# Performance work log

Measured on AMD Instinct MI355X. Metric: run time of the kernel, lower is better.

The kernel has to match this reference:

```python
import jax, jax.numpy as jnp
import numpy as np

B, S, D, H = 2, 2048, 2048, 16
HD = D // H
SCALE = 1.0 / np.sqrt(HD)


def setup_inputs() -> dict:
    key = jax.random.key(0)
    ks = jax.random.split(key, 11)
    xav = np.sqrt(6.0 / (D + D))  # xavier uniform bound for square weights
    def w(k):
        return jax.random.uniform(k, (D, D), jnp.float32, -xav, xav)
    return {
        "query": jax.random.normal(ks[0], (B, S, D), jnp.float32),
        "key": jax.random.normal(ks[1], (B, S, D), jnp.float32),
        "value": jax.random.normal(ks[2], (B, S, D), jnp.float32),
        "Wq": w(ks[3]), "bq": jnp.zeros((D,), jnp.float32),
        "Wk": w(ks[4]), "bk": jnp.zeros((D,), jnp.float32),
        "Wv": w(ks[5]), "bv": jnp.zeros((D,), jnp.float32),
        "Wo": w(ks[6]), "bo": jnp.zeros((D,), jnp.float32),
    }


def reference(query, key, value, Wq, bq, Wk, bk, Wv, bv, Wo, bo):
    # projections (torch Linear: x @ W.T + b)
    q = query @ Wq.T + bq
    k = key @ Wk.T + bk
    v = value @ Wv.T + bv
    # [B, H, S, HD]
    q = q.reshape(B, S, H, HD).transpose(0, 2, 1, 3)
    k = k.reshape(B, S, H, HD).transpose(0, 2, 1, 3)
    v = v.reshape(B, S, H, HD).transpose(0, 2, 1, 3)
    scores = jnp.einsum("bhqd,bhkd->bhqk", q, k) * SCALE
    causal = jnp.triu(jnp.ones((S, S), bool), k=1)
    scores = jnp.where(causal, -jnp.inf, scores)
    attn = jax.nn.softmax(scores, axis=-1)  # dropout p=0.0 -> identity
    out = jnp.einsum("bhqk,bhkd->bhqd", attn, v)
    out = out.transpose(0, 2, 1, 3).reshape(B, S, D)
    return out @ Wo.T + bo
```

## Files before the change

### kernel.cpp

```cpp
#include <hip/hip_runtime.h>
#include <hip/hip_bf16.h>


#define LOG2E 1.44269504088896340736f

typedef __attribute__((ext_vector_type(8))) short short8;
typedef __attribute__((ext_vector_type(4))) short short4b;
typedef __attribute__((ext_vector_type(4))) float floatx4;

__device__ __forceinline__ short f2bf(float f) {
  unsigned int u = __builtin_bit_cast(unsigned int, f);
  u += 0x7FFFu + ((u >> 16) & 1u);
  return (short)(u >> 16);
}

__device__ __forceinline__ short8 cvt8(float4 f0, float4 f1) {
  return (short8){f2bf(f0.x), f2bf(f0.y), f2bf(f0.z), f2bf(f0.w),
                  f2bf(f1.x), f2bf(f1.y), f2bf(f1.z), f2bf(f1.w)};
}

__device__ __forceinline__ short4b pack4bf(float a, float b, float c, float d) {
  __hip_bfloat162 lo = __float22bfloat162_rn(float2{a, b});
  __hip_bfloat162 hi = __float22bfloat162_rn(float2{c, d});
  short4b r;
  r[0] = __builtin_bit_cast(short, lo.x); r[1] = __builtin_bit_cast(short, lo.y);
  r[2] = __builtin_bit_cast(short, hi.x); r[3] = __builtin_bit_cast(short, hi.y);
  return r;
}

__device__ __forceinline__ void gl_lds16(const void* g, void* l) {
  __builtin_amdgcn_global_load_lds(
      (const __attribute__((address_space(1))) unsigned int*)g,
      (__attribute__((address_space(3))) unsigned int*)l, 16, 0, 0);
}

__global__ __launch_bounds__(256) void cvt7_k(
    const float* __restrict__ s0, const float* __restrict__ s1,
    const float* __restrict__ s2, const float* __restrict__ s3,
    const float* __restrict__ s4, const float* __restrict__ s5,
    const float* __restrict__ s6,
    unsigned short* __restrict__ d0, unsigned short* __restrict__ d1,
    unsigned short* __restrict__ d2, unsigned short* __restrict__ d3,
    unsigned short* __restrict__ d4, unsigned short* __restrict__ d5,
    unsigned short* __restrict__ d6, int nAct, int nW)
{
  const float* s; unsigned short* d; int n;
  switch (blockIdx.y) {
    case 0: s = s0; d = d0; n = nAct; break;
    case 1: s = s1; d = d1; n = nAct; break;
    case 2: s = s2; d = d2; n = nAct; break;
    case 3: s = s3; d = d3; n = nW; break;
    case 4: s = s4; d = d4; n = nW; break;
    case 5: s = s5; d = d5; n = nW; break;
    default: s = s6; d = d6; n = nW; break;
  }
  const long i = ((long)blockIdx.x * 256 + threadIdx.x) * 8;
  if (i >= n) return;
  float4 a = *(const float4*)(s + i);
  float4 b = *(const float4*)(s + i + 4);
  *(short8*)(d + i) = cvt8(a, b);
}

#define GEMM_CORE(A_, Bt_)                                                     \
  const unsigned short* gA[4]; int lAo[4];                                     \
  const unsigned short* gB[2]; int lBo[2];                                     \
  _Pragma("unroll")                                                            \
  for (int j = 0; j < 4; ++j) {                                                \
    const int pa = ((j >> 1) * 16 + wave * 2 + (j & 1)) * 64 + lane;           \
    const int r = pa >> 3, cp = pa & 7, cs = cp ^ (r & 7);                     \
    gA[j]  = A_ + (bm + r) * (long)K + cs * 8;                                 \
    lAo[j] = pa * 8;                                                           \
  }                                                                            \
  _Pragma("unroll")                                                            \
  for (int j = 0; j < 2; ++j) {                                                \
    const int pb = (wave * 2 + j) * 64 + lane;                                 \
    const int r = pb >> 3, cp = pb & 7, cs = cp ^ (r & 7);                     \
    gB[j]  = Bt_ + (bn + r) * (long)K + cs * 8;                                \
    lBo[j] = pb * 8;                                                           \
  }                                                                            \
  floatx4 acc[4][4];                                                           \
  _Pragma("unroll")                                                            \
  for (int i = 0; i < 4; ++i)                                                  \
    _Pragma("unroll")                                                          \
    for (int j = 0; j < 4; ++j) acc[i][j] = (floatx4){0.f, 0.f, 0.f, 0.f};     \
  const int NT = K >> 6;                                                       \
  _Pragma("unroll")                                                            \
  for (int j = 0; j < 4; ++j) gl_lds16(gA[j], &As[0][lAo[j]]);                 \
  _Pragma("unroll")                                                            \
  for (int j = 0; j < 2; ++j) gl_lds16(gB[j], &Bs[0][lBo[j]]);                 \
  if (NT > 1) {                                                                \
    _Pragma("unroll")                                                          \
    for (int j = 0; j < 4; ++j) gl_lds16(gA[j] + 64, &As[1][lAo[j]]);          \
    _Pragma("unroll")                                                          \
    for (int j = 0; j < 2; ++j) gl_lds16(gB[j] + 64, &Bs[1][lBo[j]]);          \
    asm volatile("s_waitcnt vmcnt(6)" ::: "memory");                           \
  } else {                                                                     \
    asm volatile("s_waitcnt vmcnt(0)" ::: "memory");                           \
  }                                                                            \
  __builtin_amdgcn_s_barrier();                                                \
  int cur3 = 0;                                                                \
  for (int t = 0; t < NT; ++t) {                                               \
    int nx2 = cur3 + 2; if (nx2 >= 3) nx2 -= 3;                                \
    const long kk2 = (long)(t + 2) * 64;                                       \
    const bool st2 = (t + 2) < NT;                                             \
    const bool st1 = (t + 1) < NT;                                             \
    const unsigned short* Ab = As[cur3];                                       \
    const unsigned short* Bb = Bs[cur3];                                       \
                            \
    short8 af0[4], bf0[4], af1[4], bf1[4];                                     \
    _Pragma("unroll")                                                          \
    for (int mt = 0; mt < 4; ++mt)                                             \
      af0[mt] = *(const short8*)&Ab[(wm * 64 + mt * 16 + l16) * 64 +           \
                                    ((quad ^ lx7) * 8)];                       \
    _Pragma("unroll")                                                          \
    for (int nt = 0; nt < 4; ++nt)                                             \
      bf0[nt] = *(const short8*)&Bb[(wn * 64 + nt * 16 + l16) * 64 +           \
                                    ((quad ^ lx7) * 8)];                       \
    _Pragma("unroll")                                                          \
    for (int mt = 0; mt < 4; ++mt)                                             \
      af1[mt] = *(const short8*)&Ab[(wm * 64 + mt * 16 + l16) * 64 +           \
                                    (((4 + quad) ^ lx7) * 8)];                 \
    _Pragma("unroll")                                                          \
    for (int nt = 0; nt < 4; ++nt)                                             \
      bf1[nt] = *(const short8*)&Bb[(wn * 64 + nt * 16 + l16) * 64 +           \
                                    (((4 + quad) ^ lx7) * 8)];                 \
    if (st2) { gl_lds16(gA[0] + kk2, &As[nx2][lAo[0]]);                        \
               gl_lds16(gA[1] + kk2, &As[nx2][lAo[1]]);                        \
               gl_lds16(gA[2] + kk2, &As[nx2][lAo[2]]); }                      \
    __builtin_amdgcn_s_barrier();                                              \
                      \
    __builtin_amdgcn_s_setprio(1);                                             \
    _Pragma("unroll")                                                          \
    for (int nt = 0; nt < 4; ++nt)                                             \
      _Pragma("unroll")                                                        \
      for (int mt = 0; mt < 4; ++mt)                                           \
        acc[mt][nt] = __builtin_amdgcn_mfma_f32_16x16x32_bf16(                 \
            af0[mt], bf0[nt], acc[mt][nt], 0, 0, 0);                           \
    __builtin_amdgcn_s_setprio(0);                                             \
    __builtin_amdgcn_s_barrier();                                              \
                         \
    if (st2) { gl_lds16(gA[3] + kk2, &As[nx2][lAo[3]]);                        \
               gl_lds16(gB[0] + kk2, &Bs[nx2][lBo[0]]);                        \
               gl_lds16(gB[1] + kk2, &Bs[nx2][lBo[1]]); }                      \
    __builtin_amdgcn_s_setprio(1);                                             \
    _Pragma("unroll")                                                          \
    for (int nt = 0; nt < 4; ++nt)                                             \
      _Pragma("unroll")                                                        \
      for (int mt = 0; mt < 4; ++mt)                                           \
        acc[mt][nt] = __builtin_amdgcn_mfma_f32_16x16x32_bf16(                 \
            af1[mt], bf1[nt], acc[mt][nt], 0, 0, 0);                           \
    __builtin_amdgcn_s_setprio(0);                                             \
    if (st1) {                                                                 \
      if (st2) asm volatile("s_waitcnt vmcnt(6)" ::: "memory");                \
      else     asm volatile("s_waitcnt vmcnt(0)" ::: "memory");                \
    }                                                                          \
    __builtin_amdgcn_s_barrier();                                              \
    cur3 = cur3 + 1 >= 3 ? 0 : cur3 + 1;                                       \
  }

__global__ __launch_bounds__(512, 1) void gemmqkv_k(
    const unsigned short* __restrict__ Aq, const unsigned short* __restrict__ Ak,
    const unsigned short* __restrict__ Av,
    const unsigned short* __restrict__ Bq, const unsigned short* __restrict__ Bk,
    const unsigned short* __restrict__ Bv,
    const float* __restrict__ biq, const float* __restrict__ bik,
    const float* __restrict__ biv,
    unsigned short* __restrict__ Cq, unsigned short* __restrict__ Ck,
    unsigned short* __restrict__ Cv, float qalpha)
{
  constexpr int K = 2048, N = 2048;
  __shared__ __align__(16) unsigned short As[3][256 * 64];
  __shared__ __align__(16) unsigned short Bs[3][128 * 64];

  const int tid  = threadIdx.x;
  const int lane = tid & 63;
  const int wave = tid >> 6;
  const int quad = lane >> 4;
  const int l16  = lane & 15;
  const int lx7  = l16 & 7;
  const int wm   = wave >> 1, wn = wave & 1;

  const unsigned short* A; const unsigned short* Bt; const float* bias;
  unsigned short* C; float alpha = 1.0f; bool vt = false;
  if (blockIdx.z == 0)      { A = Aq; Bt = Bq; bias = biq; C = Cq; alpha = qalpha; }
  else if (blockIdx.z == 1) { A = Ak; Bt = Bk; bias = bik; C = Ck; }
  else                      { A = Av; Bt = Bv; bias = biv; C = Cv; vt = true; }

  const int lin  = (int)(blockIdx.y * 16 + blockIdx.x);
  const int xcd  = lin & 7;
  const int slot = lin >> 3;
  const int bx = (xcd & 1) * 8 + (slot & 7);
  const int by = (xcd >> 1) * 4 + (slot >> 3);
  const long bm = (long)by * 256;
  const long bn = (long)bx * 128;

  GEMM_CORE(A, Bt)

  if (vt) {
    __syncthreads();
    unsigned short* Ct = &As[0][0];
#pragma unroll
    for (int nt = 0; nt < 4; ++nt) {
      const int col_l = wn * 64 + nt * 16 + l16;
      const float bval = bias[bn + col_l];
#pragma unroll
      for (int mt = 0; mt < 4; ++mt) {
        const int row_l = wm * 64 + mt * 16 + quad * 4;
#pragma unroll
        for (int rg = 0; rg < 4; ++rg)
          Ct[col_l * 264 + row_l + rg] = (unsigned short)f2bf((acc[mt][nt][rg] + bval) * alpha);
      }
    }
    __syncthreads();
    const int b  = (int)(bm >> 11);
    const int s0 = (int)(bm & 2047);
    const int d   = tid >> 2;
    const int seg = tid & 3;
    unsigned short* dst = C +
        ((long)(b * 16 + bx) * 128 + d) * 2048 + s0 + seg * 64;
    const unsigned short* src = &Ct[d * 264 + seg * 64];
#pragma unroll
    for (int c = 0; c < 8; ++c)
      *(uint4*)(dst + c * 8) = *(const uint4*)(src + c * 8);
  } else {
#pragma unroll
    for (int nt = 0; nt < 4; ++nt) {
      const long col = bn + wn * 64 + nt * 16 + l16;
      const float bval = bias[col];
#pragma unroll
      for (int mt = 0; mt < 4; ++mt) {
#pragma unroll
        for (int rg = 0; rg < 4; ++rg) {
          const long row = bm + wm * 64 + mt * 16 + quad * 4 + rg;
          C[row * (long)N + col] = (unsigned short)f2bf((acc[mt][nt][rg] + bval) * alpha);
        }
      }
    }
  }
}

__global__ __launch_bounds__(512, 1) void gemmo_k(
    const unsigned short* __restrict__ A, const unsigned short* __restrict__ Bt,
    const float* __restrict__ bias, float* __restrict__ C)
{
  constexpr int K = 2048, N = 2048;
  __shared__ __align__(16) unsigned short As[3][256 * 64];
  __shared__ __align__(16) unsigned short Bs[3][128 * 64];

  const int tid  = threadIdx.x;
  const int lane = tid & 63;
  const int wave = tid >> 6;
  const int quad = lane >> 4;
  const int l16  = lane & 15;
  const int lx7  = l16 & 7;
  const int wm   = wave >> 1, wn = wave & 1;

  const int lin  = (int)(blockIdx.y * 16 + blockIdx.x);
  const int xcd  = lin & 7;
  const int slot = lin >> 3;
  const int bx = (xcd & 1) * 8 + (slot & 7);
  const int by = (xcd >> 1) * 4 + (slot >> 3);
  const long bm = (long)by * 256;
  const long bn = (long)bx * 128;

  GEMM_CORE(A, Bt)

#pragma unroll
  for (int nt = 0; nt < 4; ++nt) {
    const long col = bn + wn * 64 + nt * 16 + l16;
    const float bval = bias[col];
#pragma unroll
    for (int mt = 0; mt < 4; ++mt) {
#pragma unroll
      for (int rg = 0; rg < 4; ++rg) {
        const long row = bm + wm * 64 + mt * 16 + quad * 4 + rg;
        C[row * (long)N + col] = (acc[mt][nt][rg] + bval);
      }
    }
  }
}

template<bool A_BF16, bool OUT_BF16, bool VT_OUT>
__global__ __launch_bounds__(256, 2) void gemm_bias_k(
    const void* __restrict__ Aptr, const float* __restrict__ Bt,
    const float* __restrict__ bias, void* __restrict__ Cptr,
    int M, int N, int K, float alpha)
{
  __shared__ __align__(16) unsigned short smem[128 * 136];
  unsigned short* As = smem;
  unsigned short* Bs = smem + 128 * 40;

  const int tid  = threadIdx.x;
  const int lane = tid & 63;
  const int wave = tid >> 6;
  const int quad = lane >> 4;
  const int l16  = lane & 15;
  const int wr   = wave >> 1, wc = wave & 1;
  const long bm  = (long)blockIdx.y * 128;
  const long bn  = (long)blockIdx.x * 128;

  floatx4 acc[4][4];
#pragma unroll
  for (int i = 0; i < 4; ++i)
#pragma unroll
    for (int j = 0; j < 4; ++j) acc[i][j] = (floatx4){0.f, 0.f, 0.f, 0.f};

  const int srow = tid >> 2;
  const int cc   = tid & 3;

  for (int k0 = 0; k0 < K; k0 += 32) {
    __syncthreads();
#pragma unroll
    for (int r = 0; r < 2; ++r) {
      const int row = srow + r * 64;
      short8 av, bv;
      if (A_BF16) {
        av = *(const short8*)((const unsigned short*)Aptr + (bm + row) * (long)K + k0 + cc * 8);
      } else {
        const float* ap = (const float*)Aptr + (bm + row) * (long)K + k0 + cc * 8;
        av = cvt8(*(const float4*)ap, *(const float4*)(ap + 4));
      }
      {
        const float* bp = Bt + (bn + row) * (long)K + k0 + cc * 8;
        bv = cvt8(*(const float4*)bp, *(const float4*)(bp + 4));
      }
      *(short8*)&As[row * 40 + cc * 8] = av;
      *(short8*)&Bs[row * 40 + cc * 8] = bv;
    }
    __syncthreads();

    short8 af[4], bf[4];
#pragma unroll
    for (int t = 0; t < 4; ++t) {
      af[t] = *(const short8*)&As[(wr * 64 + t * 16 + l16) * 40 + quad * 8];
      bf[t] = *(const short8*)&Bs[(wc * 64 + t * 16 + l16) * 40 + quad * 8];
    }
#pragma unroll
    for (int mt = 0; mt < 4; ++mt)
#pragma unroll
      for (int nt = 0; nt < 4; ++nt)
        acc[mt][nt] = __builtin_amdgcn_mfma_f32_16x16x32_bf16(af[mt], bf[nt], acc[mt][nt], 0, 0, 0);
  }

  if (VT_OUT) {
    __syncthreads();
    unsigned short* Ct = smem;
#pragma unroll
    for (int nt = 0; nt < 4; ++nt) {
      const long col = bn + wc * 64 + nt * 16 + l16;
      const float bval = bias[col];
      const int col_l = wc * 64 + nt * 16 + l16;
#pragma unroll
      for (int mt = 0; mt < 4; ++mt) {
        const int row_l = wr * 64 + mt * 16 + quad * 4;
#pragma unroll
        for (int rg = 0; rg < 4; ++rg)
          Ct[col_l * 136 + row_l + rg] = (unsigned short)f2bf((acc[mt][nt][rg] + bval) * alpha);
      }
    }
    __syncthreads();
    const int b  = (int)(bm >> 11);
    const int s0 = (int)(bm & 2047);
    const int r    = tid >> 1;
    const int half = tid & 1;
    unsigned short* dst = (unsigned short*)Cptr +
        ((long)(b * 16 + blockIdx.x) * 128 + r) * 2048 + s0 + half * 64;
    const unsigned short* src = &Ct[r * 136 + half * 64];
#pragma unroll
    for (int c = 0; c < 8; ++c)
      *(uint4*)(dst + c * 8) = *(const uint4*)(src + c * 8);
  } else {
#pragma unroll
    for (int nt = 0; nt < 4; ++nt) {
      const long col = bn + wc * 64 + nt * 16 + l16;
      const float bval = bias[col];
#pragma unroll
      for (int mt = 0; mt < 4; ++mt) {
#pragma unroll
        for (int rg = 0; rg < 4; ++rg) {
          const long row = bm + wr * 64 + mt * 16 + quad * 4 + rg;
          const float v = (acc[mt][nt][rg] + bval) * alpha;
          if (OUT_BF16) ((unsigned short*)Cptr)[row * (long)N + col] = (unsigned short)f2bf(v);
          else          ((float*)Cptr)[row * (long)N + col] = v;
        }
      }
    }
  }
}

__global__ __launch_bounds__(256, 2) void flash_attn_k(
    const unsigned short* __restrict__ Q,
    const unsigned short* __restrict__ Kp,
    const unsigned short* __restrict__ Vt,
    unsigned short* __restrict__ O)
{
  constexpr int S = 2048, D = 2048, HD = 128;
  constexpr int PS = 72;

  __shared__ __align__(16) unsigned short Ks[2][64 * 128];
  __shared__ __align__(16) unsigned short Vst[2][128 * 64];
  __shared__ __align__(16) unsigned short Ps[64 * PS];

  const int tid  = threadIdx.x;
  const int lane = tid & 63;
  const int w    = tid >> 6;
  const int quad = lane >> 4;
  const int l16  = lane & 15;
  const int lx7  = l16 & 7;

  const int bx  = blockIdx.x;
  const int by  = blockIdx.y;
  const int idx = by * 2 + (bx >> 3);
  const int bh  = (bx & 7) * 4 + (idx >> 4);
  const int qsel = idx & 15;

  const long headoff = (long)(bh >> 4) * S * D + (long)(bh & 15) * HD;
  const long vtoff   = (long)bh * HD * S;

  const unsigned short* gK[4]; int oK[4];
  const unsigned short* gV[4]; int oV[4];
#pragma unroll
  for (int i = 0; i < 4; ++i) {
    const int p = (w * 4 + i) * 64 + lane;
    { const int r = p >> 4, cp = p & 15, c = cp ^ (r & 7);
      gK[i] = Kp + headoff + (long)r * D + c * 8;  oK[i] = p * 8; }
    { const int r = p >> 3, cp = p & 7, c = cp ^ (r & 7);
      gV[i] = Vt + vtoff + (long)r * S + c * 8;    oV[i] = p * 8; }
  }

#pragma unroll 1
  for (int half = 0; half < 2; ++half) {
    const int qt = half ? (31 - qsel) : qsel;
    const int qbase = qt * 64;
    const int qrow  = qbase + w * 16 + l16;
    const int qloc  = w * 16 + l16;

    short8 aq[4];
    {
      const unsigned short* qp = Q + headoff + (long)qrow * D;
#pragma unroll
      for (int ks = 0; ks < 4; ++ks)
        aq[ks] = *(const short8*)(qp + ks * 32 + quad * 8);
    }

    floatx4 o_acc[8];
#pragma unroll
    for (int t = 0; t < 8; ++t) o_acc[t] = (floatx4){0.f, 0.f, 0.f, 0.f};
    float m_i = -INFINITY;
    float l_p = 0.f;

#pragma unroll
    for (int i = 0; i < 4; ++i) gl_lds16(gK[i], &Ks[0][oK[i]]);
#pragma unroll
    for (int i = 0; i < 4; ++i) gl_lds16(gV[i], &Vst[0][oV[i]]);

    for (int kt = 0; kt <= qt; ++kt) {
      const int cur = kt & 1;
      const int kbase = kt * 64;
      if (kt < qt) {
        const long kb = (long)(kt + 1) * 64;
        const int nb = cur ^ 1;
#pragma unroll
        for (int i = 0; i < 4; ++i) gl_lds16(gK[i] + kb * D, &Ks[nb][oK[i]]);
#pragma unroll
        for (int i = 0; i < 4; ++i) gl_lds16(gV[i] + kb, &Vst[nb][oV[i]]);
        asm volatile("s_waitcnt vmcnt(8)" ::: "memory");
      } else {
        asm volatile("s_waitcnt vmcnt(0)" ::: "memory");
      }
      __builtin_amdgcn_s_barrier();

      const unsigned short* Kb = &Ks[cur][0];
      const unsigned short* Vb = &Vst[cur][0];

      floatx4 sc[4];
#pragma unroll
      for (int nt = 0; nt < 4; ++nt) sc[nt] = (floatx4){0.f, 0.f, 0.f, 0.f};
      __builtin_amdgcn_s_setprio(1);
#pragma unroll
      for (int nt = 0; nt < 4; ++nt) {
        const int krow = nt * 16 + l16;
#pragma unroll
        for (int ks = 0; ks < 4; ++ks) {
          const int cp = (ks * 4 + quad) ^ lx7;
          short8 kf = *(const short8*)&Kb[krow * 128 + cp * 8];
          sc[nt] = __builtin_amdgcn_mfma_f32_16x16x32_bf16(kf, aq[ks], sc[nt], 0, 0, 0);
        }
      }
      __builtin_amdgcn_s_setprio(0);

      float sv[4][4];
      float lmax = -INFINITY;
      if (kt == qt) {
        const int kg0 = kbase + quad * 4;
#pragma unroll
        for (int nt = 0; nt < 4; ++nt)
#pragma unroll
          for (int rg = 0; rg < 4; ++rg) {
            float v = sc[nt][rg];
            if (kg0 + nt * 16 + rg > qrow) v = -INFINITY;
            sv[nt][rg] = v;
            lmax = fmaxf(lmax, v);
          }
      } else {
#pragma unroll
        for (int nt = 0; nt < 4; ++nt)
#pragma unroll
          for (int rg = 0; rg < 4; ++rg) {
            sv[nt][rg] = sc[nt][rg];
            lmax = fmaxf(lmax, sc[nt][rg]);
          }
      }

      float al = 1.0f;
      if (__any(lmax > m_i + 8.0f)) {
        float rmax = fmaxf(lmax, __shfl_xor(lmax, 16));
        rmax = fmaxf(rmax, __shfl_xor(rmax, 32));
        const float mn = fmaxf(m_i, rmax);
        al = exp2f(m_i - mn);
        m_i = mn;
#pragma unroll
        for (int t = 0; t < 8; ++t)
#pragma unroll
          for (int rg = 0; rg < 4; ++rg) o_acc[t][rg] *= al;
      }

      float rsum = 0.f;
#pragma unroll
      for (int nt = 0; nt < 4; ++nt) {
        float p0 = exp2f(sv[nt][0] - m_i), p1 = exp2f(sv[nt][1] - m_i);
        float p2 = exp2f(sv[nt][2] - m_i), p3 = exp2f(sv[nt][3] - m_i);
        rsum += (p0 + p1) + (p2 + p3);
        *(short4b*)&Ps[qloc * PS + nt * 16 + quad * 4] = pack4bf(p0, p1, p2, p3);
      }
      l_p = l_p * al + rsum;

      short8 pf[2];
#pragma unroll
      for (int ks = 0; ks < 2; ++ks)
        pf[ks] = *(const short8*)&Ps[qloc * PS + ks * 32 + quad * 8];

      __builtin_amdgcn_s_setprio(1);
#pragma unroll
      for (int t = 0; t < 8; ++t) {
        const int drow = t * 16 + l16;
#pragma unroll
        for (int ks = 0; ks < 2; ++ks) {
          const int cp = (ks * 4 + quad) ^ lx7;
          short8 vf = *(const short8*)&Vb[drow * 64 + cp * 8];
          o_acc[t] = __builtin_amdgcn_mfma_f32_16x16x32_bf16(vf, pf[ks], o_acc[t], 0, 0, 0);
        }
      }
      __builtin_amdgcn_s_setprio(0);
      __builtin_amdgcn_s_barrier();
    }

    float l_i = l_p + __shfl_xor(l_p, 16);
    l_i += __shfl_xor(l_i, 32);
    const float rl = 1.0f / l_i;
    unsigned short* op = O + headoff + (long)qrow * D;
#pragma unroll
    for (int t = 0; t < 8; ++t) {
      *(short4b*)(op + t * 16 + quad * 4) =
          pack4bf(o_acc[t][0] * rl, o_acc[t][1] * rl, o_acc[t][2] * rl, o_acc[t][3] * rl);
    }
  }
}

extern "C" void kernel_launch(void* const* d_in, const int* in_sizes, int n_in,
                              void* d_out, int out_size, void* d_ws, size_t ws_size,
                              hipStream_t stream) {
  const float* query = (const float*)d_in[0];
  const float* key_  = (const float*)d_in[1];
  const float* value = (const float*)d_in[2];
  const float* Wq = (const float*)d_in[3];
  const float* bq = (const float*)d_in[4];
  const float* Wk = (const float*)d_in[5];
  const float* bk = (const float*)d_in[6];
  const float* Wv = (const float*)d_in[7];
  const float* bv = (const float*)d_in[8];
  const float* Wo = (const float*)d_in[9];
  const float* bo = (const float*)d_in[10];
  float* out = (float*)d_out;

  constexpr int Bz = 2, S = 2048, D = 2048;
  constexpr int M = Bz * S;
  constexpr long NELEM = (long)M * D;
  constexpr long WELEM = (long)D * D;

  const float qscale = 0.08838834764831845f * LOG2E;
  dim3 gridG(D / 128, M / 128);

  const size_t need_full = (size_t)(6 * NELEM + 4 * WELEM) * 2;

  if (ws_size >= need_full) {
    unsigned short* Qp  = (unsigned short*)d_ws;
    unsigned short* Kp  = Qp + NELEM;
    unsigned short* Vt  = Kp + NELEM;
    unsigned short* Xq  = Vt + NELEM;
    unsigned short* Xk  = Xq + NELEM;
    unsigned short* Xv  = Xk + NELEM;
    unsigned short* Wqb = Xv + NELEM;
    unsigned short* Wkb = Wqb + WELEM;
    unsigned short* Wvb = Wkb + WELEM;
    unsigned short* Wob = Wvb + WELEM;
    unsigned short* Oa  = Xq;

    cvt7_k<<<dim3(4096, 7), 256, 0, stream>>>(
        query, key_, value, Wq, Wk, Wv, Wo,
        Xq, Xk, Xv, Wqb, Wkb, Wvb, Wob, (int)NELEM, (int)WELEM);

    gemmqkv_k<<<dim3(16, 16, 3), 512, 0, stream>>>(
        Xq, Xk, Xv, Wqb, Wkb, Wvb, bq, bk, bv, Qp, Kp, Vt, qscale);

    flash_attn_k<<<dim3(16, 32), 256, 0, stream>>>(Qp, Kp, Vt, Oa);

    gemmo_k<<<dim3(16, 16), 512, 0, stream>>>(Oa, Wob, bo, out);
  } else {
    unsigned short* Qp = (unsigned short*)d_ws;
    unsigned short* Kp = Qp + NELEM;
    unsigned short* Vt = Kp + NELEM;
    unsigned short* Oa = Vt + NELEM;

    gemm_bias_k<false, true, false><<<gridG, 256, 0, stream>>>(query, Wq, bq, Qp, M, D, D, qscale);
    gemm_bias_k<false, true, false><<<gridG, 256, 0, stream>>>(key_,  Wk, bk, Kp, M, D, D, 1.0f);
    gemm_bias_k<false, true, true ><<<gridG, 256, 0, stream>>>(value, Wv, bv, Vt, M, D, D, 1.0f);

    flash_attn_k<<<dim3(16, 32), 256, 0, stream>>>(Qp, Kp, Vt, Oa);

    gemm_bias_k<true, false, false><<<gridG, 256, 0, stream>>>(Oa, Wo, bo, out, M, D, D, 1.0f);
  }
}
```

Measured before the change: 403.3 us.

## Single-buffer flash attention LDS, one q-tile per block, raise occupancy to 3

The flash attention kernel drops K/V double buffering in favour of single LDS buffers, cutting shared memory so launch bounds can ask for 3 blocks per CU. Each block now handles a single 64-row query tile instead of a paired light/heavy tile, and the grid becomes 8x128 with the longest causal tiles scheduled first. Loads are no longer prefetched, so each iteration waits on global memory, and the hope is that higher occupancy hides that latency. The removal of the paired-tile load balancing also depends on ordering the heaviest tiles first.

```diff
diff --git a/kernel.cpp b/kernel.cpp
--- a/kernel.cpp
+++ b/kernel.cpp
@@ -106,7 +106,6 @@
     const bool st1 = (t + 1) < NT;                                             \
     const unsigned short* Ab = As[cur3];                                       \
     const unsigned short* Bb = Bs[cur3];                                       \
-                            \
     short8 af0[4], bf0[4], af1[4], bf1[4];                                     \
     _Pragma("unroll")                                                          \
     for (int mt = 0; mt < 4; ++mt)                                             \
@@ -128,7 +127,6 @@
                gl_lds16(gA[1] + kk2, &As[nx2][lAo[1]]);                        \
                gl_lds16(gA[2] + kk2, &As[nx2][lAo[2]]); }                      \
     __builtin_amdgcn_s_barrier();                                              \
-                      \
     __builtin_amdgcn_s_setprio(1);                                             \
     _Pragma("unroll")                                                          \
     for (int nt = 0; nt < 4; ++nt)                                             \
@@ -138,7 +136,6 @@
             af0[mt], bf0[nt], acc[mt][nt], 0, 0, 0);                           \
     __builtin_amdgcn_s_setprio(0);                                             \
     __builtin_amdgcn_s_barrier();                                              \
-                         \
     if (st2) { gl_lds16(gA[3] + kk2, &As[nx2][lAo[3]]);                        \
                gl_lds16(gB[0] + kk2, &Bs[nx2][lBo[0]]);                        \
                gl_lds16(gB[1] + kk2, &Bs[nx2][lBo[1]]); }                      \
@@ -388,7 +385,7 @@
   }
 }
 
-__global__ __launch_bounds__(256, 2) void flash_attn_k(
+__global__ __launch_bounds__(256, 3) void flash_attn_k(
     const unsigned short* __restrict__ Q,
     const unsigned short* __restrict__ Kp,
     const unsigned short* __restrict__ Vt,
@@ -397,8 +394,8 @@
   constexpr int S = 2048, D = 2048, HD = 128;
   constexpr int PS = 72;
 
-  __shared__ __align__(16) unsigned short Ks[2][64 * 128];
-  __shared__ __align__(16) unsigned short Vst[2][128 * 64];
+  __shared__ __align__(16) unsigned short Ks[64 * 128];
+  __shared__ __align__(16) unsigned short Vst[128 * 64];
   __shared__ __align__(16) unsigned short Ps[64 * PS];
 
   const int tid  = threadIdx.x;
@@ -408,162 +405,142 @@
   const int l16  = lane & 15;
   const int lx7  = l16 & 7;
 
-  const int bx  = blockIdx.x;
-  const int by  = blockIdx.y;
-  const int idx = by * 2 + (bx >> 3);
-  const int bh  = (bx & 7) * 4 + (idx >> 4);
-  const int qsel = idx & 15;
+  const int bx = blockIdx.x;
+  const int by = blockIdx.y;
+  const int qt = 31 - (by >> 2);
+  const int bh = bx * 4 + (by & 3);
 
   const long headoff = (long)(bh >> 4) * S * D + (long)(bh & 15) * HD;
   const long vtoff   = (long)bh * HD * S;
 
-  const unsigned short* gK[4]; int oK[4];
-  const unsigned short* gV[4]; int oV[4];
+  const unsigned short* gK[4]; unsigned short* lK[4];
+  const unsigned short* gV[4]; unsigned short* lV[4];
 #pragma unroll
   for (int i = 0; i < 4; ++i) {
     const int p = (w * 4 + i) * 64 + lane;
     { const int r = p >> 4, cp = p & 15, c = cp ^ (r & 7);
-      gK[i] = Kp + headoff + (long)r * D + c * 8;  oK[i] = p * 8; }
+      gK[i] = Kp + headoff + (long)r * D + c * 8;  lK[i] = &Ks[p * 8]; }
     { const int r = p >> 3, cp = p & 7, c = cp ^ (r & 7);
-      gV[i] = Vt + vtoff + (long)r * S + c * 8;    oV[i] = p * 8; }
-  }
-
-#pragma unroll 1
-  for (int half = 0; half < 2; ++half) {
-    const int qt = half ? (31 - qsel) : qsel;
-    const int qbase = qt * 64;
-    const int qrow  = qbase + w * 16 + l16;
-    const int qloc  = w * 16 + l16;
-
-    short8 aq[4];
-    {
-      const unsigned short* qp = Q + headoff + (long)qrow * D;
-#pragma unroll
-      for (int ks = 0; ks < 4; ++ks)
-        aq[ks] = *(const short8*)(qp + ks * 32 + quad * 8);
-    }
-
-    floatx4 o_acc[8];
-#pragma unroll
-    for (int t = 0; t < 8; ++t) o_acc[t] = (floatx4){0.f, 0.f, 0.f, 0.f};
-    float m_i = -INFINITY;
-    float l_p = 0.f;
-
-#pragma unroll
-    for (int i = 0; i < 4; ++i) gl_lds16(gK[i], &Ks[0][oK[i]]);
-#pragma unroll
-    for (int i = 0; i < 4; ++i) gl_lds16(gV[i], &Vst[0][oV[i]]);
-
-    for (int kt = 0; kt <= qt; ++kt) {
-      const int cur = kt & 1;
-      const int kbase = kt * 64;
-      if (kt < qt) {
-        const long kb = (long)(kt + 1) * 64;
-        const int nb = cur ^ 1;
-#pragma unroll
-        for (int i = 0; i < 4; ++i) gl_lds16(gK[i] + kb * D, &Ks[nb][oK[i]]);
-#pragma unroll
-        for (int i = 0; i < 4; ++i) gl_lds16(gV[i] + kb, &Vst[nb][oV[i]]);
-        asm volatile("s_waitcnt vmcnt(8)" ::: "memory");
-      } else {
-        asm volatile("s_waitcnt vmcnt(0)" ::: "memory");
-      }
-      __builtin_amdgcn_s_barrier();
-
-      const unsigned short* Kb = &Ks[cur][0];
-      const unsigned short* Vb = &Vst[cur][0];
-
-      floatx4 sc[4];
-#pragma unroll
-      for (int nt = 0; nt < 4; ++nt) sc[nt] = (floatx4){0.f, 0.f, 0.f, 0.f};
-      __builtin_amdgcn_s_setprio(1);
-#pragma unroll
-      for (int nt = 0; nt < 4; ++nt) {
-        const int krow = nt * 16 + l16;
-#pragma unroll
-        for (int ks = 0; ks < 4; ++ks) {
-          const int cp = (ks * 4 + quad) ^ lx7;
-          short8 kf = *(const short8*)&Kb[krow * 128 + cp * 8];
-          sc[nt] = __builtin_amdgcn_mfma_f32_16x16x32_bf16(kf, aq[ks], sc[nt], 0, 0, 0);
+      gV[i] = Vt + vtoff + (long)r * S + c * 8;    lV[i] = &Vst[p * 8]; }
+  }
+
+  const int qbase = qt * 64;
+  const int qrow  = qbase + w * 16 + l16;
+  const int qloc  = w * 16 + l16;
+
+  short8 aq[4];
+  {
+    const unsigned short* qp = Q + headoff + (long)qrow * D;
+#pragma unroll
+    for (int ks = 0; ks < 4; ++ks)
+      aq[ks] = *(const short8*)(qp + ks * 32 + quad * 8);
+  }
+
+  floatx4 o_acc[8];
+#pragma unroll
+  for (int t = 0; t < 8; ++t) o_acc[t] = (floatx4){0.f, 0.f, 0.f, 0.f};
+  float m_i = -INFINITY;
+  float l_p = 0.f;
+
+  for (int kt = 0; kt <= qt; ++kt) {
+    const int kbase = kt * 64;
+#pragma unroll
+    for (int i = 0; i < 4; ++i) gl_lds16(gK[i] + (long)kbase * D, lK[i]);
+#pragma unroll
+    for (int i = 0; i < 4; ++i) gl_lds16(gV[i] + kbase, lV[i]);
+    asm volatile("s_waitcnt vmcnt(0)" ::: "memory");
+    __builtin_amdgcn_s_barrier();
+
+    floatx4 sc[4];
+#pragma unroll
+    for (int nt = 0; nt < 4; ++nt) sc[nt] = (floatx4){0.f, 0.f, 0.f, 0.f};
+    __builtin_amdgcn_s_setprio(1);
+#pragma unroll
+    for (int nt = 0; nt < 4; ++nt) {
+      const int krow = nt * 16 + l16;
+#pragma unroll
+      for (int ks = 0; ks < 4; ++ks) {
+        const int cp = (ks * 4 + quad) ^ lx7;
+        short8 kf = *(const short8*)&Ks[krow * 128 + cp * 8];
+        sc[nt] = __builtin_amdgcn_mfma_f32_16x16x32_bf16(kf, aq[ks], sc[nt], 0, 0, 0);
+      }
+    }
+    __builtin_amdgcn_s_setprio(0);
+
+    float sv[4][4];
+    float lmax = -INFINITY;
+    if (kt == qt) {
+      const int kg0 = kbase + quad * 4;
+#pragma unroll
+      for (int nt = 0; nt < 4; ++nt)
+#pragma unroll
+        for (int rg = 0; rg < 4; ++rg) {
+          float v = sc[nt][rg];
+          if (kg0 + nt * 16 + rg > qrow) v = -INFINITY;
+          sv[nt][rg] = v;
+          lmax = fmaxf(lmax, v);
         }
-      }
-      __builtin_amdgcn_s_setprio(0);
-
-      float sv[4][4];
-      float lmax = -INFINITY;
-      if (kt == qt) {
-        const int kg0 = kbase + quad * 4;
-#pragma unroll
-        for (int nt = 0; nt < 4; ++nt)
-#pragma unroll
-          for (int rg = 0; rg < 4; ++rg) {
-            float v = sc[nt][rg];
-            if (kg0 + nt * 16 + rg > qrow) v = -INFINITY;
-            sv[nt][rg] = v;
-            lmax = fmaxf(lmax, v);
-          }
-      } else {
-#pragma unroll
-        for (int nt = 0; nt < 4; ++nt)
-#pragma unroll
-          for (int rg = 0; rg < 4; ++rg) {
-            sv[nt][rg] = sc[nt][rg];
-            lmax = fmaxf(lmax, sc[nt][rg]);
-          }
-      }
-
-      float al = 1.0f;
-      if (__any(lmax > m_i + 8.0f)) {
-        float rmax = fmaxf(lmax, __shfl_xor(lmax, 16));
-        rmax = fmaxf(rmax, __shfl_xor(rmax, 32));
-        const float mn = fmaxf(m_i, rmax);
-        al = exp2f(m_i - mn);
-        m_i = mn;
-#pragma unroll
-        for (int t = 0; t < 8; ++t)
-#pragma unroll
-          for (int rg = 0; rg < 4; ++rg) o_acc[t][rg] *= al;
-      }
-
-      float rsum = 0.f;
-#pragma unroll
-      for (int nt = 0; nt < 4; ++nt) {
-        float p0 = exp2f(sv[nt][0] - m_i), p1 = exp2f(sv[nt][1] - m_i);
-        float p2 = exp2f(sv[nt][2] - m_i), p3 = exp2f(sv[nt][3] - m_i);
-        rsum += (p0 + p1) + (p2 + p3);
-        *(short4b*)&Ps[qloc * PS + nt * 16 + quad * 4] = pack4bf(p0, p1, p2, p3);
-      }
-      l_p = l_p * al + rsum;
-
-      short8 pf[2];
-#pragma unroll
-      for (int ks = 0; ks < 2; ++ks)
-        pf[ks] = *(const short8*)&Ps[qloc * PS + ks * 32 + quad * 8];
-
-      __builtin_amdgcn_s_setprio(1);
-#pragma unroll
-      for (int t = 0; t < 8; ++t) {
-        const int drow = t * 16 + l16;
-#pragma unroll
-        for (int ks = 0; ks < 2; ++ks) {
-          const int cp = (ks * 4 + quad) ^ lx7;
-          short8 vf = *(const short8*)&Vb[drow * 64 + cp * 8];
-          o_acc[t] = __builtin_amdgcn_mfma_f32_16x16x32_bf16(vf, pf[ks], o_acc[t], 0, 0, 0);
+    } else {
+#pragma unroll
+      for (int nt = 0; nt < 4; ++nt)
+#pragma unroll
+        for (int rg = 0; rg < 4; ++rg) {
+          sv[nt][rg] = sc[nt][rg];
+          lmax = fmaxf(lmax, sc[nt][rg]);
         }
-      }
-      __builtin_amdgcn_s_setprio(0);
-      __builtin_amdgcn_s_barrier();
-    }
-
-    float l_i = l_p + __shfl_xor(l_p, 16);
-    l_i += __shfl_xor(l_i, 32);
-    const float rl = 1.0f / l_i;
-    unsigned short* op = O + headoff + (long)qrow * D;
+    }
+
+    float al = 1.0f;
+    if (__any(lmax > m_i + 8.0f)) {
+      float rmax = fmaxf(lmax, __shfl_xor(lmax, 16));
+      rmax = fmaxf(rmax, __shfl_xor(rmax, 32));
+      const float mn = fmaxf(m_i, rmax);
+      al = exp2f(m_i - mn);
+      m_i = mn;
+#pragma unroll
+      for (int t = 0; t < 8; ++t)
+#pragma unroll
+        for (int rg = 0; rg < 4; ++rg) o_acc[t][rg] *= al;
+    }
+
+    float rsum = 0.f;
+#pragma unroll
+    for (int nt = 0; nt < 4; ++nt) {
+      float p0 = exp2f(sv[nt][0] - m_i), p1 = exp2f(sv[nt][1] - m_i);
+      float p2 = exp2f(sv[nt][2] - m_i), p3 = exp2f(sv[nt][3] - m_i);
+      rsum += (p0 + p1) + (p2 + p3);
+      *(short4b*)&Ps[qloc * PS + nt * 16 + quad * 4] = pack4bf(p0, p1, p2, p3);
+    }
+    l_p = l_p * al + rsum;
+
+    short8 pf[2];
+#pragma unroll
+    for (int ks = 0; ks < 2; ++ks)
+      pf[ks] = *(const short8*)&Ps[qloc * PS + ks * 32 + quad * 8];
+
+    __builtin_amdgcn_s_setprio(1);
 #pragma unroll
     for (int t = 0; t < 8; ++t) {
-      *(short4b*)(op + t * 16 + quad * 4) =
-          pack4bf(o_acc[t][0] * rl, o_acc[t][1] * rl, o_acc[t][2] * rl, o_acc[t][3] * rl);
-    }
+      const int drow = t * 16 + l16;
+#pragma unroll
+      for (int ks = 0; ks < 2; ++ks) {
+        const int cp = (ks * 4 + quad) ^ lx7;
+        short8 vf = *(const short8*)&Vst[drow * 64 + cp * 8];
+        o_acc[t] = __builtin_amdgcn_mfma_f32_16x16x32_bf16(vf, pf[ks], o_acc[t], 0, 0, 0);
+      }
+    }
+    __builtin_amdgcn_s_setprio(0);
+    __builtin_amdgcn_s_barrier();
+  }
+
+  float l_i = l_p + __shfl_xor(l_p, 16);
+  l_i += __shfl_xor(l_i, 32);
+  const float rl = 1.0f / l_i;
+  unsigned short* op = O + headoff + (long)qrow * D;
+#pragma unroll
+  for (int t = 0; t < 8; ++t) {
+    *(short4b*)(op + t * 16 + quad * 4) =
+        pack4bf(o_acc[t][0] * rl, o_acc[t][1] * rl, o_acc[t][2] * rl, o_acc[t][3] * rl);
   }
 }
 
@@ -613,7 +590,7 @@
     gemmqkv_k<<<dim3(16, 16, 3), 512, 0, stream>>>(
         Xq, Xk, Xv, Wqb, Wkb, Wvb, bq, bk, bv, Qp, Kp, Vt, qscale);
 
-    flash_attn_k<<<dim3(16, 32), 256, 0, stream>>>(Qp, Kp, Vt, Oa);
+    flash_attn_k<<<dim3(8, 128), 256, 0, stream>>>(Qp, Kp, Vt, Oa);
 
     gemmo_k<<<dim3(16, 16), 512, 0, stream>>>(Oa, Wob, bo, out);
   } else {
@@ -626,7 +603,7 @@
     gemm_bias_k<false, true, false><<<gridG, 256, 0, stream>>>(key_,  Wk, bk, Kp, M, D, D, 1.0f);
     gemm_bias_k<false, true, true ><<<gridG, 256, 0, stream>>>(value, Wv, bv, Vt, M, D, D, 1.0f);
 
-    flash_attn_k<<<dim3(16, 32), 256, 0, stream>>>(Qp, Kp, Vt, Oa);
+    flash_attn_k<<<dim3(8, 128), 256, 0, stream>>>(Qp, Kp, Vt, Oa);
 
     gemm_bias_k<true, false, false><<<gridG, 256, 0, stream>>>(Oa, Wo, bo, out, M, D, D, 1.0f);
   }
```

Measured after the change: 408.8 us. No clear change (+1.4%).
